# Optimization experiments

Measured on AMD Instinct MI355X. Metric: run time of the kernel, lower is better.

Reference implementation:

```python
import jax, jax.numpy as jnp
import numpy as np

B, T, C, H = 4, 2048, 1024, 16
HS = C // H
DFF = 4 * C
EPS = 1e-5


def setup_inputs() -> dict:
    key = jax.random.key(0)
    ks = jax.random.split(key, 8)
    s = 0.02
    inp = {
        "x": jax.random.normal(ks[0], (B, T, C), jnp.float32),
        # attention linear weights, stored (in, out) so h @ W + b
        "Wq": jax.random.normal(ks[1], (C, C), jnp.float32) * s,
        "bq": jnp.zeros((C,), jnp.float32),
        "Wk": jax.random.normal(ks[2], (C, C), jnp.float32) * s,
        "bk": jnp.zeros((C,), jnp.float32),
        "Wv": jax.random.normal(ks[3], (C, C), jnp.float32) * s,
        "bv": jnp.zeros((C,), jnp.float32),
        "Wo": jax.random.normal(ks[4], (C, C), jnp.float32) * s,
        "bo": jnp.zeros((C,), jnp.float32),
        # feed-forward
        "W1": jax.random.normal(ks[5], (C, DFF), jnp.float32) * s,
        "b1": jnp.zeros((DFF,), jnp.float32),
        "W2": jax.random.normal(ks[6], (DFF, C), jnp.float32) * s,
        "b2": jnp.zeros((C,), jnp.float32),
        # layernorms
        "g1": jnp.ones((C,), jnp.float32),
        "be1": jnp.zeros((C,), jnp.float32),
        "g2": jnp.ones((C,), jnp.float32),
        "be2": jnp.zeros((C,), jnp.float32),
    }
    return inp


def _layernorm(x, g, b):
    mu = jnp.mean(x, axis=-1, keepdims=True)
    var = jnp.mean(jnp.square(x - mu), axis=-1, keepdims=True)
    return (x - mu) * jax.lax.rsqrt(var + EPS) * g + b


def _attention(h, Wq, bq, Wk, bk, Wv, bv, Wo, bo):
    Bx, Tx, Cx = h.shape
    q = (h @ Wq + bq).reshape(Bx, Tx, H, HS).transpose(0, 2, 1, 3)  # [B,H,T,hs]
    k = (h @ Wk + bk).reshape(Bx, Tx, H, HS).transpose(0, 2, 1, 3)
    v = (h @ Wv + bv).reshape(Bx, Tx, H, HS).transpose(0, 2, 1, 3)
    att = jnp.einsum("bhqd,bhkd->bhqk", q, k) * (1.0 / np.sqrt(HS))
    causal = jnp.tril(jnp.ones((Tx, Tx), bool))
    att = jnp.where(causal, att, jnp.float32(-jnp.inf))
    att = jax.nn.softmax(att, axis=-1)
    y = jnp.einsum("bhqk,bhkd->bhqd", att, v)
    y = y.transpose(0, 2, 1, 3).reshape(Bx, Tx, Cx)
    return y @ Wo + bo


def reference(x, Wq, bq, Wk, bk, Wv, bv, Wo, bo, W1, b1, W2, b2, g1, be1, g2, be2):
    x = x + _attention(_layernorm(x, g1, be1), Wq, bq, Wk, bk, Wv, bv, Wo, bo)
    h = _layernorm(x, g2, be2)
    ff = jax.nn.relu(h @ W1 + b1) @ W2 + b2
    return x + ff
```

## Files before the change

### kernel.cpp

```cpp
#include <hip/hip_runtime.h>
#include <hip/hip_bf16.h>

#define Bq   4
#define Tq   2048
#define Cq   1024
#define Hq   16
#define HSq  64
#define DFFq 4096
#define Mq   (Bq*Tq)

typedef float f32x4  __attribute__((ext_vector_type(4)));
typedef short bf16x8 __attribute__((ext_vector_type(8)));

__device__ __forceinline__ float b2f(unsigned short u){ return __uint_as_float(((unsigned)u)<<16); }
__device__ __forceinline__ unsigned short f2b(float f){
  union { __hip_bfloat16 h; unsigned short u; } cv;
  cv.h = __float2bfloat16(f);
  return cv.u;
}
__device__ __forceinline__ unsigned pkbf(float a, float b){
  const unsigned ua = __float_as_uint(a) + 0x8000u;
  const unsigned ub = __float_as_uint(b) + 0x8000u;
  return (ua>>16) | (ub & 0xffff0000u);
}

__device__ __forceinline__ void gld_lds16(const unsigned short* g, unsigned short* l){
  __builtin_amdgcn_global_load_lds(
      (const __attribute__((address_space(1))) void*)g,
      (__attribute__((address_space(3))) void*)l, 16, 0, 0);
}

__device__ __forceinline__ int probe_bf16(const unsigned short* w){
  const int lane = threadIdx.x & 63;
  ushort4 u = *(const ushort4*)(w + lane*4);
  int cnt = 0;
  {
    unsigned e;
    e=(u.x>>7)&0xFF; cnt += (e>=0x60 && e<=0x7E);
    e=(u.y>>7)&0xFF; cnt += (e>=0x60 && e<=0x7E);
    e=(u.z>>7)&0xFF; cnt += (e>=0x60 && e<=0x7E);
    e=(u.w>>7)&0xFF; cnt += (e>=0x60 && e<=0x7E);
  }
#pragma unroll
  for (int off=1; off<64; off<<=1) cnt += __shfl_xor(cnt, off, 64);
  return cnt >= 224;
}

__global__ __launch_bounds__(256) void cvtvec_k(
    const void* s0,const void* s1,const void* s2,const void* s3,const void* s4,
    const void* s5,const void* s6,const void* s7,const void* s8,const void* s9,
    const unsigned short* __restrict__ probew, unsigned short* __restrict__ dst)
{
  const int isbf = probe_bf16(probew);
  const int idx = blockIdx.x*256 + threadIdx.x;
  const int seg = idx>>12, off = idx&4095;
  const void* s; int len;
  switch(seg){
    case 0: s=s0; len=1024; break;
    case 1: s=s1; len=1024; break;
    case 2: s=s2; len=1024; break;
    case 3: s=s3; len=1024; break;
    case 4: s=s4; len=4096; break;
    case 5: s=s5; len=1024; break;
    case 6: s=s6; len=1024; break;
    case 7: s=s7; len=1024; break;
    case 8: s=s8; len=1024; break;
    default: s=s9; len=1024; break;
  }
  if (off >= len) return;
  const float v = isbf ? b2f(((const unsigned short*)s)[off]) : ((const float*)s)[off];
  dst[idx] = f2b(v);
}

__global__ __launch_bounds__(256) void ln_k(const void* __restrict__ xin,
    const unsigned short* __restrict__ g, const unsigned short* __restrict__ be,
    unsigned short* __restrict__ out, const unsigned short* __restrict__ probew)
{
  const int isbf = probe_bf16(probew);
  const int row = blockIdx.x;
  const int tid = threadIdx.x;
  float v[4];
  if (isbf){
    const unsigned short* xr = (const unsigned short*)xin + (size_t)row*Cq;
    ushort4 u = *(const ushort4*)(xr + tid*4);
    v[0]=b2f(u.x); v[1]=b2f(u.y); v[2]=b2f(u.z); v[3]=b2f(u.w);
  } else {
    const float* xr = (const float*)xin + (size_t)row*Cq;
    float4 u = *(const float4*)(xr + tid*4);
    v[0]=u.x; v[1]=u.y; v[2]=u.z; v[3]=u.w;
  }
  float s  = v[0]+v[1]+v[2]+v[3];
  float ss = v[0]*v[0]+v[1]*v[1]+v[2]*v[2]+v[3]*v[3];
#pragma unroll
  for (int off=32; off>0; off>>=1){
    s  += __shfl_down(s,  off, 64);
    ss += __shfl_down(ss, off, 64);
  }
  __shared__ float sa[4], sb[4];
  const int wave = tid>>6, lane = tid&63;
  if (lane==0){ sa[wave]=s; sb[wave]=ss; }
  __syncthreads();
  s  = sa[0]+sa[1]+sa[2]+sa[3];
  ss = sb[0]+sb[1]+sb[2]+sb[3];
  const float mu  = s  * (1.0f/Cq);
  const float var = ss * (1.0f/Cq) - mu*mu;
  const float rs  = rsqrtf(fmaxf(var, 0.0f) + 1e-5f);
  ushort4 o; unsigned short* op = (unsigned short*)&o;
#pragma unroll
  for (int i=0;i<4;i++){
    const int ci = tid*4+i;
    op[i] = f2b((v[i]-mu)*rs*b2f(g[ci]) + b2f(be[ci]));
  }
  *(ushort4*)(out + (size_t)row*Cq + tid*4) = o;
}

__global__ __launch_bounds__(256) void wtrans4_k(
    const void* __restrict__ w0, const void* __restrict__ w1,
    const void* __restrict__ w2, const void* __restrict__ w3,
    unsigned short* __restrict__ Wqkv, unsigned short* __restrict__ WoT,
    const unsigned short* __restrict__ probew)
{
  const int isbf = probe_bf16(probew);
  const int z = blockIdx.z;
  const void* Win = (z==0)?w0 : (z==1)?w1 : (z==2)?w2 : w3;
  unsigned short* Wt = (z<3) ? (Wqkv + (size_t)z*1048576) : WoT;
  __shared__ __align__(16) unsigned short tile[64][72];
  const int kb = blockIdx.x, nb = blockIdx.y, tid = threadIdx.x;
#pragma unroll
  for (int i=0;i<2;i++){
    const int v = tid + i*256;
    const int kr = v>>3, nc = (v&7)*8;
    if (isbf){
      *(uint4*)&tile[kr][nc] =
        *(const uint4*)((const unsigned short*)Win + (size_t)(kb*64+kr)*1024 + nb*64 + nc);
    } else {
      const float* wp = (const float*)Win + (size_t)(kb*64+kr)*1024 + nb*64 + nc;
      float4 a = *(const float4*)wp, b = *(const float4*)(wp+4);
      alignas(16) unsigned short t[8] =
        {f2b(a.x),f2b(a.y),f2b(a.z),f2b(a.w),f2b(b.x),f2b(b.y),f2b(b.z),f2b(b.w)};
      *(uint4*)&tile[kr][nc] = *(const uint4*)t;
    }
  }
  __syncthreads();
#pragma unroll
  for (int i=0;i<2;i++){
    const int v = tid + i*256;
    const int nr = v>>3, kc = (v&7)*8;
    alignas(16) unsigned short tmp[8];
#pragma unroll
    for (int j=0;j<8;j++) tmp[j] = tile[kc+j][nr];
    *(uint4*)(Wt + (size_t)(nb*64+nr)*1024 + kb*64 + kc) = *(const uint4*)tmp;
  }
}

__global__ __launch_bounds__(256) void wtrans_k(const void* __restrict__ Win,
    unsigned short* __restrict__ Wt, const int Kd, const int Nd,
    const unsigned short* __restrict__ probew)
{
  const int isbf = probe_bf16(probew);
  __shared__ __align__(16) unsigned short tile[64][72];
  const int kb = blockIdx.x, nb = blockIdx.y, tid = threadIdx.x;
#pragma unroll
  for (int i=0;i<2;i++){
    const int v = tid + i*256;
    const int kr = v>>3, nc = (v&7)*8;
    if (isbf){
      *(uint4*)&tile[kr][nc] =
        *(const uint4*)((const unsigned short*)Win + (size_t)(kb*64+kr)*Nd + nb*64 + nc);
    } else {
      const float* wp = (const float*)Win + (size_t)(kb*64+kr)*Nd + nb*64 + nc;
      float4 a = *(const float4*)wp, b = *(const float4*)(wp+4);
      alignas(16) unsigned short t[8] =
        {f2b(a.x),f2b(a.y),f2b(a.z),f2b(a.w),f2b(b.x),f2b(b.y),f2b(b.z),f2b(b.w)};
      *(uint4*)&tile[kr][nc] = *(const uint4*)t;
    }
  }
  __syncthreads();
#pragma unroll
  for (int i=0;i<2;i++){
    const int v = tid + i*256;
    const int nr = v>>3, kc = (v&7)*8;
    alignas(16) unsigned short tmp[8];
#pragma unroll
    for (int j=0;j<8;j++) tmp[j] = tile[kc+j][nr];
    *(uint4*)(Wt + (size_t)(nb*64+nr)*Kd + kb*64 + kc) = *(const uint4*)tmp;
  }
}

template<int RELU, int RESMODE, int OUTMODE>
__global__ __launch_bounds__(256,2) void gemm_bt(
    const unsigned short* __restrict__ A,
    const unsigned short* __restrict__ Bt,
    const unsigned short* __restrict__ bias,
    const void* resid, void* outp,
    const int N, const int K, const int lda, const int ldb,
    const unsigned short* __restrict__ probew)
{
  int isbf = 1;
  if constexpr (OUTMODE==1 || OUTMODE==5 || RESMODE==2) isbf = probe_bf16(probew);

  int koff = 0;
  int kTiles = K >> 6;
  if constexpr (OUTMODE==5){
    if (isbf){
      if (blockIdx.z) return;
      kTiles = K >> 5;
    } else {
      koff = blockIdx.z * K;
    }
  }

  __shared__ __align__(16) unsigned short Al[128][64];
  __shared__ __align__(16) unsigned short Bl[128][64];
  const int tid  = threadIdx.x;
  const int lane = tid & 63, wave = tid >> 6;
  const int qd   = lane >> 4, c = lane & 15;
  const int m0   = blockIdx.x * 128, n0 = blockIdx.y * 128;
  const int wm   = (wave & 1) * 64, wn = (wave >> 1) * 64;
  const int srow = tid >> 3;
  const int pg   = tid & 7;

  const f32x4 zf = {0.f,0.f,0.f,0.f};
  f32x4 acc[4][4];
#pragma unroll
  for (int i=0;i<4;i++)
#pragma unroll
    for (int j=0;j<4;j++) acc[i][j] = zf;

  for (int kt=0; kt<kTiles; ++kt){
    const int k0 = koff + kt*64;
#pragma unroll
    for (int i=0;i<4;i++){
      const int row = i*32 + srow;
      const int lg  = (pg + row) & 7;
      gld_lds16(A  + (size_t)(m0+row)*lda + k0 + lg*8, &Al[row][pg*8]);
      gld_lds16(Bt + (size_t)(n0+row)*ldb + k0 + lg*8, &Bl[row][pg*8]);
    }
    __syncthreads();
#pragma unroll
    for (int ks=0; ks<2; ++ks){
      const int rg = ((ks*4+qd-c)&7)*8;
      bf16x8 af[4], bfr[4];
#pragma unroll
      for (int mt=0;mt<4;mt++) af[mt]  = *(const bf16x8*)&Al[wm+mt*16+c][rg];
#pragma unroll
      for (int nt=0;nt<4;nt++) bfr[nt] = *(const bf16x8*)&Bl[wn+nt*16+c][rg];
#pragma unroll
      for (int mt=0;mt<4;mt++)
#pragma unroll
        for (int nt=0;nt<4;nt++)
          acc[mt][nt] = __builtin_amdgcn_mfma_f32_16x16x32_bf16(af[mt], bfr[nt], acc[mt][nt], 0,0,0);
    }
    __syncthreads();
  }

  float bv[4];
  if constexpr (OUTMODE==3){
    const int segn = (n0+wn) >> 10;
    const unsigned short* bseg = bias + segn*4096;
#pragma unroll
    for (int nt=0;nt<4;nt++) bv[nt] = b2f(bseg[(n0+wn+nt*16+c)&1023]);
  } else {
#pragma unroll
    for (int nt=0;nt<4;nt++) bv[nt] = b2f(bias[n0+wn+nt*16+c]);
  }

#pragma unroll
  for (int mt=0;mt<4;mt++){
#pragma unroll
    for (int r=0;r<4;r++){
      const int m = m0 + wm + mt*16 + qd*4 + r;
#pragma unroll
      for (int nt=0;nt<4;nt++){
        const int n = n0 + wn + nt*16 + c;
        float val = acc[mt][nt][r] + ((OUTMODE==5 && !isbf && blockIdx.z!=0) ? 0.0f : bv[nt]);
        if (RELU) val = fmaxf(val, 0.0f);
        if constexpr (RESMODE==2){
          const size_t idx = (size_t)m*N + n;
          val += isbf ? b2f(((const unsigned short*)resid)[idx])
                      : ((const float*)resid)[idx];
        }
        if constexpr (OUTMODE==3){
          const int segn = (n0+wn) >> 10;
          const int n1 = n & 1023;
          unsigned short* dst = (unsigned short*)outp + (size_t)segn*8388608;
          if (segn < 2){
            dst[(size_t)m*1024 + n1] = f2b(val);
          } else {
            const size_t vidx = ((size_t)((m>>11)*16 + (n1>>6))*64 + (n1&63))*Tq + (m&2047);
            dst[vidx] = f2b(val);
          }
        } else if constexpr (OUTMODE==5){
          const size_t idx = (size_t)m*N + n;
          if (!isbf){
            atomicAdd((float*)outp + idx, val);
          } else {
            unsigned short* o16 = (unsigned short*)outp;
            o16[idx] = f2b(val + b2f(o16[idx]));
          }
        } else if constexpr (OUTMODE==1){
          const size_t idx = (size_t)m*N + n;
          if (isbf) ((unsigned short*)outp)[idx] = f2b(val);
          else      ((float*)outp)[idx] = val;
        } else {
          ((unsigned short*)outp)[(size_t)m*N + n] = f2b(val);
        }
      }
    }
  }
}

__global__ __launch_bounds__(256,3) void attn_k(const unsigned short* __restrict__ Qg,
    const unsigned short* __restrict__ Kg, const unsigned short* __restrict__ Vt,
    unsigned short* __restrict__ Y)
{
  const int bh = blockIdx.x;
  const int jq = (int)(gridDim.y - 1) - blockIdx.y;
  const int b = bh >> 4, h = bh & 15;
  const int tid = threadIdx.x, lane = tid & 63, wave = tid >> 6;
  const int qd = lane >> 4, c = lane & 15;
  const int q0  = jq * 128;
  const int wq0 = q0 + wave * 32;
  __shared__ __align__(16) unsigned short Kl[64*64];
  __shared__ __align__(16) unsigned short Vl[64*64];
  __shared__ __align__(16) unsigned short Pl[4][32][72];

  bf16x8 qf[2][2];
#pragma unroll
  for (int nt=0; nt<2; ++nt)
#pragma unroll
    for (int h2=0; h2<2; ++h2)
      qf[nt][h2] = *(const bf16x8*)(Qg + ((size_t)b*Tq + wq0 + nt*16 + c)*Cq
                                       + h*HSq + h2*32 + qd*8);

  const f32x4 zf = {0.f,0.f,0.f,0.f};
  const float NEG = -1.0e30f;
  f32x4 o[2][4];
  float lacc[2] = {0.f, 0.f};
#pragma unroll
  for (int nt=0;nt<2;nt++)
#pragma unroll
    for (int dt=0;dt<4;dt++) o[nt][dt]=zf;
  const float SCL = 0.125f * 1.44269504088896340736f;

  const int stg_r  = (lane>>3);
  const int stg_pg = lane & 7;

  const int r_row = (wave*2)*8 + stg_r;
  const unsigned short* kp0 = Kg + ((size_t)b*Tq + r_row)*Cq + h*HSq + ((stg_pg + r_row)&7)*8;
  const unsigned short* kp1 = Kg + ((size_t)b*Tq + r_row+8)*Cq + h*HSq + ((stg_pg + r_row+8)&7)*8;
  const unsigned short* vp0 = Vt + ((size_t)bh*HSq + r_row)*Tq + ((stg_pg + r_row)&7)*8;
  const unsigned short* vp1 = Vt + ((size_t)bh*HSq + r_row+8)*Tq + ((stg_pg + r_row+8)&7)*8;
  unsigned short* kl0 = &Kl[(r_row  )*64 + stg_pg*8];
  unsigned short* kl1 = &Kl[(r_row+8)*64 + stg_pg*8];
  unsigned short* vl0 = &Vl[(r_row  )*64 + stg_pg*8];
  unsigned short* vl1 = &Vl[(r_row+8)*64 + stg_pg*8];

  const int nkt = 2*(jq+1);
  for (int kt=0; kt<nkt; ++kt){
    const int k0 = kt*64;
    gld_lds16(kp0, kl0);  gld_lds16(kp1, kl1);
    gld_lds16(vp0, vl0);  gld_lds16(vp1, vl1);
    kp0 += 64*Cq; kp1 += 64*Cq; vp0 += 64; vp1 += 64;
    __syncthreads();

    if (k0 <= wq0 + 31){
      bf16x8 kf[4][2], vf[4][2];
#pragma unroll
      for (int mt=0;mt<4;mt++)
#pragma unroll
        for (int h2=0;h2<2;h2++){
          kf[mt][h2] = *(const bf16x8*)&Kl[(mt*16+c)*64 + ((h2*4+qd-c)&7)*8];
          vf[mt][h2] = *(const bf16x8*)&Vl[(mt*16+c)*64 + ((h2*4+qd-c)&7)*8];
        }
      const int domask = (k0 + 63 > wq0) ? 1 : 0;
#pragma unroll
      for (int nt=0; nt<2; ++nt){
        const int query = wq0 + nt*16 + c;
        f32x4 s[4];
#pragma unroll
        for (int mt=0;mt<4;mt++){
          f32x4 sa = zf;
          sa = __builtin_amdgcn_mfma_f32_16x16x32_bf16(kf[mt][0], qf[nt][0], sa, 0,0,0);
          sa = __builtin_amdgcn_mfma_f32_16x16x32_bf16(kf[mt][1], qf[nt][1], sa, 0,0,0);
          s[mt] = sa;
        }
        float p[4][4];
        float rs = 0.f;
#pragma unroll
        for (int mt=0;mt<4;mt++)
#pragma unroll
          for (int r=0;r<4;r++){
            float xv = fminf(s[mt][r]*SCL, 80.0f);
            if (domask && (k0 + mt*16 + qd*4 + r > query)) xv = NEG;
            const float pe = exp2f(xv);
            p[mt][r] = pe;
            rs += pe;
          }
        lacc[nt] += rs;
#pragma unroll
        for (int mt=0;mt<4;mt++){
          uint2 w2v;
          w2v.x = pkbf(p[mt][0], p[mt][1]);
          w2v.y = pkbf(p[mt][2], p[mt][3]);
          *(uint2*)&Pl[wave][nt*16+c][mt*16+qd*4] = w2v;
        }
        bf16x8 pf0 = *(const bf16x8*)&Pl[wave][nt*16+c][qd*8];
        bf16x8 pf1 = *(const bf16x8*)&Pl[wave][nt*16+c][32+qd*8];
#pragma unroll
        for (int dt=0;dt<4;dt++){
          o[nt][dt] = __builtin_amdgcn_mfma_f32_16x16x32_bf16(vf[dt][0], pf0, o[nt][dt], 0,0,0);
          o[nt][dt] = __builtin_amdgcn_mfma_f32_16x16x32_bf16(vf[dt][1], pf1, o[nt][dt], 0,0,0);
        }
      }
    }
    __syncthreads();
  }

#pragma unroll
  for (int nt=0;nt<2;nt++){
    lacc[nt] += __shfl_xor(lacc[nt], 16, 64);
    lacc[nt] += __shfl_xor(lacc[nt], 32, 64);
  }
#pragma unroll
  for (int nt=0;nt<2;nt++){
    const float inv = 1.0f / lacc[nt];
#pragma unroll
    for (int dt=0;dt<4;dt++){
      uint2 w2v;
      w2v.x = pkbf(o[nt][dt][0]*inv, o[nt][dt][1]*inv);
      w2v.y = pkbf(o[nt][dt][2]*inv, o[nt][dt][3]*inv);
      *(uint2*)&Pl[wave][nt*16+c][dt*16+qd*4] = w2v;
    }
  }
#pragma unroll
  for (int pass=0; pass<4; ++pass){
    const int qrow = pass*8 + (lane>>3);
    const int dcol = (lane&7)*8;
    uint4 val = *(const uint4*)&Pl[wave][qrow][dcol];
    *(uint4*)(Y + ((size_t)b*Tq + wq0 + qrow)*Cq + h*HSq + dcol) = val;
  }
}

extern "C" void kernel_launch(void* const* d_in, const int* in_sizes, int n_in,
                              void* d_out, int out_size, void* d_ws, size_t ws_size,
                              hipStream_t stream)
{
  (void)in_sizes; (void)n_in; (void)out_size; (void)ws_size;
  const void* x   = d_in[0];
  const void* Wq  = d_in[1];
  const void* Wk  = d_in[3];
  const void* Wv  = d_in[5];
  const void* Wo  = d_in[7];
  const void* W1  = d_in[9];
  const void* W2  = d_in[11];
  const unsigned short* pw = (const unsigned short*)W1;

  char* ws = (char*)d_ws;
  const size_t MB = 1u<<20;
  unsigned short* W1T   = (unsigned short*)(ws + 0*MB);
  unsigned short* W2T   = (unsigned short*)(ws + 8*MB);
  unsigned short* WqkvT = (unsigned short*)(ws + 16*MB);
  unsigned short* WoT   = (unsigned short*)(ws + 22*MB);
  unsigned short* Qb    = (unsigned short*)(ws + 24*MB);
  unsigned short* Kb    = (unsigned short*)(ws + 40*MB);
  unsigned short* Vt    = (unsigned short*)(ws + 56*MB);
  unsigned short* ff1   = (unsigned short*)(ws + 16*MB);
  unsigned short* hy    = (unsigned short*)(ws + 80*MB);
  unsigned short* vec   = (unsigned short*)(ws + 96*MB);
  unsigned short* vbo = vec + 12288;
  unsigned short* vb1 = vec + 16384;  unsigned short* vb2 = vec + 20480;
  unsigned short* vg1 = vec + 24576;  unsigned short* vbe1= vec + 28672;
  unsigned short* vg2 = vec + 32768;  unsigned short* vbe2= vec + 36864;

  const dim3 blk(256,1,1);

  cvtvec_k<<<dim3(160), blk, 0, stream>>>(d_in[2], d_in[4], d_in[6], d_in[8],
      d_in[10], d_in[12], d_in[13], d_in[14], d_in[15], d_in[16], pw, vec);

  wtrans4_k<<<dim3(16,16,4), blk, 0, stream>>>(Wq, Wk, Wv, Wo, WqkvT, WoT, pw);
  wtrans_k<<<dim3(16,64), blk, 0, stream>>>(W1, W1T, 1024, 4096, pw);
  wtrans_k<<<dim3(64,16), blk, 0, stream>>>(W2, W2T, 4096, 1024, pw);

  ln_k<<<dim3(Mq), blk, 0, stream>>>(x, vg1, vbe1, hy, pw);

  gemm_bt<0,0,3><<<dim3(64,24), blk, 0, stream>>>(hy, WqkvT, vec, nullptr, Qb,
      3072, 1024, 1024, 1024, pw);

  attn_k<<<dim3(64,16), blk, 0, stream>>>(Qb, Kb, Vt, hy);

  gemm_bt<0,2,1><<<dim3(64,8), blk, 0, stream>>>(hy, WoT, vbo, x, d_out,
      1024, 1024, 1024, 1024, pw);

  ln_k<<<dim3(Mq), blk, 0, stream>>>(d_out, vg2, vbe2, hy, pw);

  gemm_bt<1,0,0><<<dim3(64,32), blk, 0, stream>>>(hy, W1T, vb1, nullptr, ff1,
      4096, 1024, 1024, 1024, pw);
  gemm_bt<0,0,5><<<dim3(64,8,2), blk, 0, stream>>>(ff1, W2T, vb2, nullptr, d_out,
      1024, 2048, 4096, 4096, pw);
}
```

Baseline: 518.8 us.

## Switch GEMMs to 256x128 tiles with triple-buffered async LDS pipeline

Replaces the 128x128 GEMM with a 512-thread kernel computing 256x128 tiles, using three LDS stages so global-to-LDS loads for tile T+2 overlap MFMA work on tile T. Explicit vmcnt waits replace the per-iteration double __syncthreads, and s_setprio raises priority around the MFMA bursts. The larger tile improves reuse of B loads but halves the block count and uses about 144KB of LDS, limiting occupancy to one block per CU.

```diff
diff --git a/kernel.cpp b/kernel.cpp
--- a/kernel.cpp
+++ b/kernel.cpp
@@ -188,7 +188,7 @@
 }
 
 template<int RELU, int RESMODE, int OUTMODE>
-__global__ __launch_bounds__(256,2) void gemm_bt(
+__global__ __launch_bounds__(512,2) void gemm256(
     const unsigned short* __restrict__ A,
     const unsigned short* __restrict__ Bt,
     const unsigned short* __restrict__ bias,
@@ -200,26 +200,44 @@
   if constexpr (OUTMODE==1 || OUTMODE==5 || RESMODE==2) isbf = probe_bf16(probew);
 
   int koff = 0;
-  int kTiles = K >> 6;
+  int nT = K >> 6;
   if constexpr (OUTMODE==5){
     if (isbf){
       if (blockIdx.z) return;
-      kTiles = K >> 5;
+      nT = K >> 5;
     } else {
       koff = blockIdx.z * K;
     }
   }
 
-  __shared__ __align__(16) unsigned short Al[128][64];
-  __shared__ __align__(16) unsigned short Bl[128][64];
+  __shared__ __align__(16) unsigned short Al[3][256][64];
+  __shared__ __align__(16) unsigned short Bl[3][128][64];
+
   const int tid  = threadIdx.x;
   const int lane = tid & 63, wave = tid >> 6;
   const int qd   = lane >> 4, c = lane & 15;
-  const int m0   = blockIdx.x * 128, n0 = blockIdx.y * 128;
-  const int wm   = (wave & 1) * 64, wn = (wave >> 1) * 64;
+  const int m0   = blockIdx.x * 256, n0 = blockIdx.y * 128;
+  const int wm   = (wave & 3) * 64;
+  const int wn   = (wave >> 2) * 64;
   const int srow = tid >> 3;
   const int pg   = tid & 7;
 
+  auto STAGE = [&](int t, int slot){
+    const int k0 = koff + t*64;
+#pragma unroll
+    for (int i=0;i<4;i++){
+      const int row = i*64 + srow;
+      const int lg  = (pg + row) & 7;
+      gld_lds16(A  + (size_t)(m0+row)*lda + k0 + lg*8, &Al[slot][row][pg*8]);
+    }
+#pragma unroll
+    for (int i=0;i<2;i++){
+      const int row = i*64 + srow;
+      const int lg  = (pg + row) & 7;
+      gld_lds16(Bt + (size_t)(n0+row)*ldb + k0 + lg*8, &Bl[slot][row][pg*8]);
+    }
+  };
+
   const f32x4 zf = {0.f,0.f,0.f,0.f};
   f32x4 acc[4][4];
 #pragma unroll
@@ -227,31 +245,56 @@
 #pragma unroll
     for (int j=0;j<4;j++) acc[i][j] = zf;
 
-  for (int kt=0; kt<kTiles; ++kt){
-    const int k0 = koff + kt*64;
-#pragma unroll
-    for (int i=0;i<4;i++){
-      const int row = i*32 + srow;
-      const int lg  = (pg + row) & 7;
-      gld_lds16(A  + (size_t)(m0+row)*lda + k0 + lg*8, &Al[row][pg*8]);
-      gld_lds16(Bt + (size_t)(n0+row)*ldb + k0 + lg*8, &Bl[row][pg*8]);
-    }
-    __syncthreads();
-#pragma unroll
-    for (int ks=0; ks<2; ++ks){
-      const int rg = ((ks*4+qd-c)&7)*8;
-      bf16x8 af[4], bfr[4];
-#pragma unroll
-      for (int mt=0;mt<4;mt++) af[mt]  = *(const bf16x8*)&Al[wm+mt*16+c][rg];
-#pragma unroll
-      for (int nt=0;nt<4;nt++) bfr[nt] = *(const bf16x8*)&Bl[wn+nt*16+c][rg];
-#pragma unroll
-      for (int mt=0;mt<4;mt++)
-#pragma unroll
-        for (int nt=0;nt<4;nt++)
-          acc[mt][nt] = __builtin_amdgcn_mfma_f32_16x16x32_bf16(af[mt], bfr[nt], acc[mt][nt], 0,0,0);
-    }
-    __syncthreads();
+  STAGE(0,0);
+  if (nT > 1) STAGE(1,1);
+
+  const int rg0 = ((qd     - c) & 7) * 8;
+  const int rg1 = ((4 + qd - c) & 7) * 8;
+
+  int s = 0;
+  for (int T=0; T<nT; ++T){
+    if (T+1 < nT) { asm volatile("s_waitcnt vmcnt(6)" ::: "memory"); }
+    else          { asm volatile("s_waitcnt vmcnt(0)" ::: "memory"); }
+    __builtin_amdgcn_s_barrier();
+    asm volatile("" ::: "memory");
+
+    const unsigned short (*As)[64] = Al[s];
+    const unsigned short (*Bs)[64] = Bl[s];
+
+    bf16x8 af0[4], bf0[4];
+#pragma unroll
+    for (int mt=0;mt<4;mt++) af0[mt] = *(const bf16x8*)&As[wm+mt*16+c][rg0];
+#pragma unroll
+    for (int nt=0;nt<4;nt++) bf0[nt] = *(const bf16x8*)&Bs[wn+nt*16+c][rg0];
+
+    if (T+2 < nT){
+      const int ss = (s==0) ? 2 : s-1;
+      STAGE(T+2, ss);
+    }
+
+    __builtin_amdgcn_s_setprio(1);
+#pragma unroll
+    for (int mt=0;mt<4;mt++)
+#pragma unroll
+      for (int nt=0;nt<4;nt++)
+        acc[mt][nt] = __builtin_amdgcn_mfma_f32_16x16x32_bf16(af0[mt], bf0[nt], acc[mt][nt], 0,0,0);
+    __builtin_amdgcn_s_setprio(0);
+
+    bf16x8 af1[4], bf1[4];
+#pragma unroll
+    for (int mt=0;mt<4;mt++) af1[mt] = *(const bf16x8*)&As[wm+mt*16+c][rg1];
+#pragma unroll
+    for (int nt=0;nt<4;nt++) bf1[nt] = *(const bf16x8*)&Bs[wn+nt*16+c][rg1];
+
+    __builtin_amdgcn_s_setprio(1);
+#pragma unroll
+    for (int mt=0;mt<4;mt++)
+#pragma unroll
+      for (int nt=0;nt<4;nt++)
+        acc[mt][nt] = __builtin_amdgcn_mfma_f32_16x16x32_bf16(af1[mt], bf1[nt], acc[mt][nt], 0,0,0);
+    __builtin_amdgcn_s_setprio(0);
+
+    s = (s==2) ? 0 : s+1;
   }
 
   float bv[4];
@@ -474,6 +517,7 @@
   unsigned short* vg2 = vec + 32768;  unsigned short* vbe2= vec + 36864;
 
   const dim3 blk(256,1,1);
+  const dim3 blk512(512,1,1);
 
   cvtvec_k<<<dim3(160), blk, 0, stream>>>(d_in[2], d_in[4], d_in[6], d_in[8],
       d_in[10], d_in[12], d_in[13], d_in[14], d_in[15], d_in[16], pw, vec);
@@ -484,18 +528,18 @@
 
   ln_k<<<dim3(Mq), blk, 0, stream>>>(x, vg1, vbe1, hy, pw);
 
-  gemm_bt<0,0,3><<<dim3(64,24), blk, 0, stream>>>(hy, WqkvT, vec, nullptr, Qb,
+  gemm256<0,0,3><<<dim3(32,24), blk512, 0, stream>>>(hy, WqkvT, vec, nullptr, Qb,
       3072, 1024, 1024, 1024, pw);
 
   attn_k<<<dim3(64,16), blk, 0, stream>>>(Qb, Kb, Vt, hy);
 
-  gemm_bt<0,2,1><<<dim3(64,8), blk, 0, stream>>>(hy, WoT, vbo, x, d_out,
+  gemm256<0,2,1><<<dim3(32,8), blk512, 0, stream>>>(hy, WoT, vbo, x, d_out,
       1024, 1024, 1024, 1024, pw);
 
   ln_k<<<dim3(Mq), blk, 0, stream>>>(d_out, vg2, vbe2, hy, pw);
 
-  gemm_bt<1,0,0><<<dim3(64,32), blk, 0, stream>>>(hy, W1T, vb1, nullptr, ff1,
+  gemm256<1,0,0><<<dim3(32,32), blk512, 0, stream>>>(hy, W1T, vb1, nullptr, ff1,
       4096, 1024, 1024, 1024, pw);
-  gemm_bt<0,0,5><<<dim3(64,8,2), blk, 0, stream>>>(ff1, W2T, vb2, nullptr, d_out,
+  gemm256<0,0,5><<<dim3(32,8,2), blk512, 0, stream>>>(ff1, W2T, vb2, nullptr, d_out,
       1024, 2048, 4096, 4096, pw);
 }
```

Result: slower. 555.4 us (+7.0%).

## Double-buffer K/V tiles in attention kernel to overlap loads with compute

Applied to the files above, without the earlier changes.

Doubles the shared-memory K and V tiles in the causal attention kernel. The next K/V tile is now prefetched into the alternate buffer right after a single barrier, while MFMA work runs on the current buffer. The goal is to hide global-to-LDS load latency and drop one of the two barriers per key tile. The cost is about 16 KB more LDS per block, which could reduce occupancy below the declared three blocks per CU.

```diff
diff --git a/kernel.cpp b/kernel.cpp
--- a/kernel.cpp
+++ b/kernel.cpp
@@ -321,8 +321,8 @@
   const int qd = lane >> 4, c = lane & 15;
   const int q0  = jq * 128;
   const int wq0 = q0 + wave * 32;
-  __shared__ __align__(16) unsigned short Kl[64*64];
-  __shared__ __align__(16) unsigned short Vl[64*64];
+  __shared__ __align__(16) unsigned short Kl[2][64*64];
+  __shared__ __align__(16) unsigned short Vl[2][64*64];
   __shared__ __align__(16) unsigned short Pl[4][32][72];
 
   bf16x8 qf[2][2];
@@ -346,23 +346,30 @@
   const int stg_r  = (lane>>3);
   const int stg_pg = lane & 7;
 
-  const int r_row = (wave*2)*8 + stg_r;
-  const unsigned short* kp0 = Kg + ((size_t)b*Tq + r_row)*Cq + h*HSq + ((stg_pg + r_row)&7)*8;
-  const unsigned short* kp1 = Kg + ((size_t)b*Tq + r_row+8)*Cq + h*HSq + ((stg_pg + r_row+8)&7)*8;
-  const unsigned short* vp0 = Vt + ((size_t)bh*HSq + r_row)*Tq + ((stg_pg + r_row)&7)*8;
-  const unsigned short* vp1 = Vt + ((size_t)bh*HSq + r_row+8)*Tq + ((stg_pg + r_row+8)&7)*8;
-  unsigned short* kl0 = &Kl[(r_row  )*64 + stg_pg*8];
-  unsigned short* kl1 = &Kl[(r_row+8)*64 + stg_pg*8];
-  unsigned short* vl0 = &Vl[(r_row  )*64 + stg_pg*8];
-  unsigned short* vl1 = &Vl[(r_row+8)*64 + stg_pg*8];
+  const int r_row = wave*16 + stg_r;
+  const int sw0 = ((stg_pg + r_row  )&7)*8;
+  const int sw1 = ((stg_pg + r_row+8)&7)*8;
+  const unsigned short* kbase0 = Kg + ((size_t)b*Tq + r_row  )*Cq + h*HSq + sw0;
+  const unsigned short* kbase1 = Kg + ((size_t)b*Tq + r_row+8)*Cq + h*HSq + sw1;
+  const unsigned short* vbase0 = Vt + ((size_t)bh*HSq + r_row  )*Tq + sw0;
+  const unsigned short* vbase1 = Vt + ((size_t)bh*HSq + r_row+8)*Tq + sw1;
+
+  auto stageKV = [&](int kt, int buf){
+    const size_t koffK = (size_t)kt*64*Cq;
+    const int    koffV = kt*64;
+    gld_lds16(kbase0 + koffK, &Kl[buf][(r_row  )*64 + stg_pg*8]);
+    gld_lds16(kbase1 + koffK, &Kl[buf][(r_row+8)*64 + stg_pg*8]);
+    gld_lds16(vbase0 + koffV, &Vl[buf][(r_row  )*64 + stg_pg*8]);
+    gld_lds16(vbase1 + koffV, &Vl[buf][(r_row+8)*64 + stg_pg*8]);
+  };
 
   const int nkt = 2*(jq+1);
+  stageKV(0, 0);
+  int cur = 0;
   for (int kt=0; kt<nkt; ++kt){
+    __syncthreads();
+    if (kt+1 < nkt) stageKV(kt+1, cur^1);
     const int k0 = kt*64;
-    gld_lds16(kp0, kl0);  gld_lds16(kp1, kl1);
-    gld_lds16(vp0, vl0);  gld_lds16(vp1, vl1);
-    kp0 += 64*Cq; kp1 += 64*Cq; vp0 += 64; vp1 += 64;
-    __syncthreads();
 
     if (k0 <= wq0 + 31){
       bf16x8 kf[4][2], vf[4][2];
@@ -370,8 +377,8 @@
       for (int mt=0;mt<4;mt++)
 #pragma unroll
         for (int h2=0;h2<2;h2++){
-          kf[mt][h2] = *(const bf16x8*)&Kl[(mt*16+c)*64 + ((h2*4+qd-c)&7)*8];
-          vf[mt][h2] = *(const bf16x8*)&Vl[(mt*16+c)*64 + ((h2*4+qd-c)&7)*8];
+          kf[mt][h2] = *(const bf16x8*)&Kl[cur][(mt*16+c)*64 + ((h2*4+qd-c)&7)*8];
+          vf[mt][h2] = *(const bf16x8*)&Vl[cur][(mt*16+c)*64 + ((h2*4+qd-c)&7)*8];
         }
       const int domask = (k0 + 63 > wq0) ? 1 : 0;
 #pragma unroll
@@ -414,7 +421,7 @@
         }
       }
     }
-    __syncthreads();
+    cur ^= 1;
   }
 
 #pragma unroll
```

New measurement: 525.1 us. Within noise of the previous version (+1.2%).
